# Kernel optimization log

Hardware: AMD Instinct MI355X
Metric: run time of the kernel (lower is better)

## Reference

```python
import jax, jax.numpy as jnp
import numpy as np

BINS = 256
EPS = 1e-8


def _norm255(x):
    # (x - min) / (max - min) * 255, truncated to int (torch .int())
    mx = jnp.max(x, axis=(2, 3), keepdims=True)
    mn = jnp.min(x, axis=(2, 3), keepdims=True)
    return ((x - mn) / (mx - mn) * 255.0).astype(jnp.int32)


def _hist256(x):
    # x int32 [B,C,H,W] -> per-(b,c) 256-bin histogram [B,C,256] float32
    B, C = x.shape[0], x.shape[1]
    flat = x.reshape(B * C, -1)
    rows = jnp.arange(B * C)[:, None]
    h = jnp.zeros((B * C, BINS), jnp.float32).at[rows, flat].add(1.0)
    return h.reshape(B, C, BINS)


def _entropy(x):
    # faithful to Entropy(): p = hist / (H*W); h = -sum p*log(p+1e-8)
    B, C, H, W = x.shape
    p = _hist256(x) / (H * W)
    h = -jnp.sum(p * jnp.log(p + EPS), axis=2)
    return h[:, :, None, None]  # [B,C,1,1]


def _joint_entropy(x_p, x_ms):
    # Faithful to Joint_entropy's quirky count: for each (i,j) it counts pixels
    # where (x_ms==i AND x_p==j) OR (x_ms!=i AND x_p!=j).
    # count[i,j] = 2*J[i,j] + npix - hist_ms[i] - hist_p[j], J = joint histogram.
    B, C, H, W = x_ms.shape
    npix = H * W
    bins = jnp.arange(BINS)
    M = (x_ms.reshape(B, C, npix)[..., None] == bins).astype(jnp.float32)  # [B,C,P,256]
    P = (x_p.reshape(B, npix)[..., None] == bins).astype(jnp.float32)      # [B,P,256]
    J = jnp.einsum('bcpi,bpj->bcij', M, P)                                  # [B,C,256,256]
    hist_ms = jnp.sum(M, axis=2)  # [B,C,256]
    hist_p = jnp.sum(P, axis=1)   # [B,256]
    count = 2.0 * J + npix - hist_ms[:, :, :, None] - hist_p[:, None, None, :]
    p = count / float(BINS * BINS)  # original divides by 256*256, not npix
    h = -jnp.sum(p * jnp.log(p + EPS), axis=(2, 3))
    return h[:, :, None, None]  # [B,C,1,1]


def _channel(f_p, f_ms):
    B, C, H, W = f_p.shape
    f_p_m = jnp.mean(f_p, axis=1, keepdims=True)  # [B,1,H,W]
    # AdaptiveAvgPool2d((16,16)) with H,W divisible by 16 == block mean
    pooled = f_p.reshape(B, C, 16, H // 16, 16, W // 16).mean(axis=(3, 5))
    f_p_a = jnp.mean(pooled, axis=1, keepdims=True)  # [B,1,16,16]
    f_ms_n = _norm255(f_ms)
    f_p_m_n = _norm255(f_p_m)
    f_p_a_n = _norm255(f_p_a)
    h_ms = _entropy(f_ms_n)                 # [B,C,1,1]
    h_p = _entropy(f_p_m_n)                 # [B,1,1,1]
    h_ms_p = _joint_entropy(f_p_a_n, f_ms_n)  # [B,C,1,1]
    mi = h_p + h_ms - h_ms_p
    mi = jax.nn.softmax(mi, axis=1)  # nn.Softmax() on 4D -> dim=1
    return f_ms + f_ms * mi


def _similarity(f_p, f_ms):
    B, C, H, W = f_p.shape
    f_ms_u = jax.image.resize(f_ms, (B, C, H, W), method='bilinear')
    a = f_ms_u.reshape(B, C, -1)
    b = f_p.reshape(B, C, -1)
    a = a - jnp.mean(a, axis=2, keepdims=True)
    b = b - jnp.mean(b, axis=2, keepdims=True)
    na = jnp.sqrt(jnp.sum(a * a, axis=2))  # [B,C] (ms norms)
    nb = jnp.sqrt(jnp.sum(b * b, axis=2))  # [B,C] (p norms)
    s = jnp.einsum('bcp,bdp->bcd', a, b)   # [B,C,C]
    return s / ((na * nb) / 100.0)[:, :, None]


def _spatial(f_p, f_ms):
    B, C, H, W = f_p.shape
    s_m = _similarity(f_p, f_ms)
    mx = jnp.max(s_m, axis=2)        # [B,C]
    idx = jnp.argmax(s_m, axis=2)    # [B,C] best f_p channel per ms channel
    scores = jax.nn.softmax(mx, axis=1)
    brow = jnp.arange(B)[:, None]
    # group score: sum of softmax scores of ms-channels that picked value v
    g = jnp.zeros((B, C), scores.dtype).at[brow, idx].add(scores)
    cnt = jnp.zeros((B, C), jnp.int32).at[brow, idx].add(1)
    k = jnp.min(jnp.sum(cnt > 0, axis=1))  # min #unique over batch
    min_k = (k + 1) // 2                   # ceil(min_k / 2)
    order = jnp.argsort(-g, axis=1)        # descending group score; absent groups (0) sort last
    sorted_scores = jnp.take_along_axis(g, order, axis=1)  # [B,C]
    pos_mask = jnp.arange(C) < min_k       # keep top min_k positions
    z = jnp.where(pos_mask[None, :], sorted_scores, -jnp.inf)
    w = jax.nn.softmax(z, axis=1)          # softmax over selected scores, 0 elsewhere
    gathered = jnp.take_along_axis(f_p, order[:, :, None, None], axis=1)  # [B,C,H,W]
    mask = jnp.sum(w[:, :, None, None] * jax.nn.sigmoid(gathered), axis=1, keepdims=True)
    return f_p + f_p * mask


def setup_inputs() -> dict:
    key = jax.random.key(0)
    k1, k2 = jax.random.split(key)
    f_p = jax.random.normal(k1, (8, 64, 256, 256), dtype=jnp.float32)
    f_ms = jax.random.normal(k2, (8, 64, 16, 16), dtype=jnp.float32)
    return {"f_p": f_p, "f_ms": f_ms}


def reference(f_p, f_ms):
    rel_ms = _channel(f_p, f_ms)
    rel_p = _spatial(f_p, f_ms)
    return (rel_p, rel_ms)
```

## Files before the change

### kernel.cpp

```cpp
#include <hip/hip_runtime.h>

#define BB 8
#define CC 64
#define HP 256
#define WP 256
#define PP 65536
#define QQ 256

__device__ __forceinline__ unsigned encF(float f) {
    unsigned u = __float_as_uint(f);
    return (u & 0x80000000u) ? ~u : (u | 0x80000000u);
}
__device__ __forceinline__ float decF(unsigned u) {
    unsigned b = (u & 0x80000000u) ? (u ^ 0x80000000u) : ~u;
    return __uint_as_float(b);
}

__device__ __forceinline__ double blockSumD(double v, double* red4) {
    int t = threadIdx.x;
    for (int d = 32; d; d >>= 1) v += __shfl_down(v, d, 64);
    __syncthreads();
    if ((t & 63) == 0) red4[t >> 6] = v;
    __syncthreads();
    double r = red4[0] + red4[1] + red4[2] + red4[3];
    __syncthreads();
    return r;
}

__global__ void k0_init(unsigned* minmax, int* histpm) {
    int t = threadIdx.x + blockIdx.x * blockDim.x;
    if (t < BB) { minmax[2 * t] = 0xFFFFFFFFu; minmax[2 * t + 1] = 0u; }
    if (t < BB * 256) histpm[t] = 0;
}

__global__ __launch_bounds__(256) void k1_fpm(const float* __restrict__ fp,
                                              float* __restrict__ fpm,
                                              unsigned* __restrict__ minmax) {
    int b = blockIdx.y;
    int i4 = blockIdx.x * 256 + threadIdx.x;
    const float4* src = (const float4*)(fp + (size_t)b * CC * PP);
    float sx = 0.f, sy = 0.f, sz = 0.f, sw = 0.f;
#pragma unroll 8
    for (int c = 0; c < CC; ++c) {
        float4 v = src[(size_t)c * (PP / 4) + i4];
        sx += v.x; sy += v.y; sz += v.z; sw += v.w;
    }
    const float inv = 1.0f / 64.0f;
    float4 m; m.x = sx * inv; m.y = sy * inv; m.z = sz * inv; m.w = sw * inv;
    ((float4*)(fpm + (size_t)b * PP))[i4] = m;
    float mn = fminf(fminf(m.x, m.y), fminf(m.z, m.w));
    float mx = fmaxf(fmaxf(m.x, m.y), fmaxf(m.z, m.w));
    for (int d = 32; d; d >>= 1) {
        mn = fminf(mn, __shfl_down(mn, d, 64));
        mx = fmaxf(mx, __shfl_down(mx, d, 64));
    }
    __shared__ unsigned smn, smx;
    if (threadIdx.x == 0) { smn = 0xFFFFFFFFu; smx = 0u; }
    __syncthreads();
    if ((threadIdx.x & 63) == 0) { atomicMin(&smn, encF(mn)); atomicMax(&smx, encF(mx)); }
    __syncthreads();
    if (threadIdx.x == 0) { atomicMin(&minmax[2 * b], smn); atomicMax(&minmax[2 * b + 1], smx); }
}

__global__ __launch_bounds__(256) void k2a_hist(const float* __restrict__ fpm,
                                                const unsigned* __restrict__ minmax,
                                                int* __restrict__ histpm) {
    int b = blockIdx.y;
    __shared__ int h[256];
    h[threadIdx.x] = 0;
    __syncthreads();
    float mn = decF(minmax[2 * b]);
    float mx = decF(minmax[2 * b + 1]);
    float dd = mx - mn;
    int i4 = blockIdx.x * 256 + threadIdx.x;
    float4 v = ((const float4*)(fpm + (size_t)b * PP))[i4];
    int b0 = (int)((v.x - mn) / dd * 255.0f);
    int b1 = (int)((v.y - mn) / dd * 255.0f);
    int b2 = (int)((v.z - mn) / dd * 255.0f);
    int b3 = (int)((v.w - mn) / dd * 255.0f);
    b0 = min(max(b0, 0), 255); b1 = min(max(b1, 0), 255);
    b2 = min(max(b2, 0), 255); b3 = min(max(b3, 0), 255);
    atomicAdd(&h[b0], 1); atomicAdd(&h[b1], 1);
    atomicAdd(&h[b2], 1); atomicAdd(&h[b3], 1);
    __syncthreads();
    atomicAdd(&histpm[b * 256 + threadIdx.x], h[threadIdx.x]);
}

__global__ __launch_bounds__(256) void k2b_entropy(const int* __restrict__ histpm,
                                                   float* __restrict__ hpE) {
    __shared__ double red4[4];
    int b = blockIdx.x;
    int n = histpm[b * 256 + threadIdx.x];
    float p = (float)n * (1.0f / 65536.0f);
    double term = -(double)(p * __logf(p + 1e-8f));
    double h = blockSumD(term, red4);
    if (threadIdx.x == 0) hpE[b] = (float)h;
}

__global__ __launch_bounds__(256) void k3_chan(const float* __restrict__ fp,
                                               float* __restrict__ cellsum,
                                               float* __restrict__ gtent,
                                               float* __restrict__ chsum,
                                               float* __restrict__ chsumsq) {
    int blk = blockIdx.x, b = blk >> 6, c = blk & 63;
    int x = threadIdx.x, s = x >> 4, r = x & 15;
    const float* src = fp + (size_t)(b * CC + c) * PP;
    __shared__ float tentL[256];
    __shared__ double red4[4];
    tentL[x] = 0.0f;
    __syncthreads();
    float wm, w0, wp;
    if (x <= 7)        { wm = 0.f; w0 = 1.f; wp = 0.f; }
    else if (x >= 248) { wm = 0.f; w0 = 1.f; wp = 0.f; }
    else if (r < 8)    { float fx = ((float)r + 8.5f) * 0.0625f; wm = 1.f - fx; w0 = fx;       wp = 0.f; }
    else               { float fx = ((float)r - 7.5f) * 0.0625f; wm = 0.f;      w0 = 1.f - fx; wp = fx;  }
    double sum = 0.0, ssq = 0.0;
    for (int q = 0; q < 16; ++q) {
        float am = 0.f, a0 = 0.f, ap = 0.f, cs = 0.f;
#pragma unroll
        for (int ry = 0; ry < 16; ++ry) {
            float v = src[(q * 16 + ry) * 256 + x];
            sum += (double)v;
            ssq += (double)v * (double)v;
            cs  += v;
            if ((q == 0 && ry < 8) || (q == 15 && ry >= 8)) {
                a0 += v;
            } else if (ry < 8) {
                float fy = ((float)ry + 8.5f) * 0.0625f;
                am += (1.f - fy) * v; a0 += fy * v;
            } else {
                float fy = ((float)ry - 7.5f) * 0.0625f;
                a0 += (1.f - fy) * v; ap += fy * v;
            }
        }
        float vals[10];
        vals[0] = am * wm; vals[1] = am * w0; vals[2] = am * wp;
        vals[3] = a0 * wm; vals[4] = a0 * w0; vals[5] = a0 * wp;
        vals[6] = ap * wm; vals[7] = ap * w0; vals[8] = ap * wp;
        vals[9] = cs;
#pragma unroll
        for (int d = 8; d; d >>= 1) {
#pragma unroll
            for (int k2 = 0; k2 < 10; ++k2) vals[k2] += __shfl_down(vals[k2], d, 16);
        }
        if (r == 0) {
            if (q > 0) {
                if (s > 0)  atomicAdd(&tentL[(q - 1) * 16 + (s - 1)], vals[0]);
                atomicAdd(&tentL[(q - 1) * 16 + s], vals[1]);
                if (s < 15) atomicAdd(&tentL[(q - 1) * 16 + (s + 1)], vals[2]);
            }
            if (s > 0)  atomicAdd(&tentL[q * 16 + (s - 1)], vals[3]);
            atomicAdd(&tentL[q * 16 + s], vals[4]);
            if (s < 15) atomicAdd(&tentL[q * 16 + (s + 1)], vals[5]);
            if (q < 15) {
                if (s > 0)  atomicAdd(&tentL[(q + 1) * 16 + (s - 1)], vals[6]);
                atomicAdd(&tentL[(q + 1) * 16 + s], vals[7]);
                if (s < 15) atomicAdd(&tentL[(q + 1) * 16 + (s + 1)], vals[8]);
            }
            cellsum[(size_t)(b * CC + c) * QQ + q * 16 + s] = vals[9];
        }
    }
    __syncthreads();
    gtent[(size_t)(b * CC + c) * QQ + x] = tentL[x];
    double st = blockSumD(sum, red4);
    double sq = blockSumD(ssq, red4);
    if (x == 0) { chsum[b * CC + c] = (float)st; chsumsq[b * CC + c] = (float)sq; }
}

__global__ __launch_bounds__(256) void k4_ms(const float* __restrict__ fms,
                                             int* __restrict__ msn,
                                             int* __restrict__ histms,
                                             float* __restrict__ hmsE,
                                             float* __restrict__ naArr,
                                             float* __restrict__ mssum) {
    int blk = blockIdx.x, b = blk >> 6, c = blk & 63, t = threadIdx.x;
    __shared__ float m[256];
    __shared__ int hist[256];
    __shared__ double red4[4];
    __shared__ double U[256];
    __shared__ unsigned umn, umx;
    float v = fms[(size_t)(b * CC + c) * QQ + t];
    m[t] = v;
    hist[t] = 0;
    if (t == 0) { umn = 0xFFFFFFFFu; umx = 0u; }
    float mn = v, mx = v;
    for (int d = 32; d; d >>= 1) {
        mn = fminf(mn, __shfl_down(mn, d, 64));
        mx = fmaxf(mx, __shfl_down(mx, d, 64));
    }
    __syncthreads();
    if ((t & 63) == 0) { atomicMin(&umn, encF(mn)); atomicMax(&umx, encF(mx)); }
    __syncthreads();
    mn = decF(umn); mx = decF(umx);
    int bin = (int)((v - mn) / (mx - mn) * 255.0f);
    bin = min(max(bin, 0), 255);
    msn[(size_t)(b * CC + c) * QQ + t] = bin;
    atomicAdd(&hist[bin], 1);
    __syncthreads();
    histms[(size_t)(b * CC + c) * QQ + t] = hist[t];
    float pf = (float)hist[t] * (1.0f / 256.0f);
    double term = -(double)(pf * __logf(pf + 1e-8f));
    double h = blockSumD(term, red4);
    if (t == 0) hmsE[b * CC + c] = (float)h;
    int i = t >> 4, j = t & 15;
    double kdj = (j == 0 || j == 15) ? 13.328125 : 10.65625;
    double mv = (double)m[t];
    double uu = kdj * mv + 2.671875 * ((j > 0 ? (double)m[t - 1] : 0.0) +
                                       (j < 15 ? (double)m[t + 1] : 0.0));
    U[t] = uu;
    __syncthreads();
    double kdi = (i == 0 || i == 15) ? 13.328125 : 10.65625;
    double vv = kdi * U[t] + 2.671875 * ((i > 0 ? U[t - 16] : 0.0) +
                                         (i < 15 ? U[t + 16] : 0.0));
    double sq = blockSumD(mv * vv, red4);
    double msm = blockSumD(mv, red4);
    if (t == 0) {
        mssum[b * CC + c] = (float)msm;
        double meanu = msm * (1.0 / 256.0);
        double na2 = sq - 65536.0 * meanu * meanu;
        naArr[b * CC + c] = (float)sqrt(na2 > 0.0 ? na2 : 0.0);
    }
}

__global__ __launch_bounds__(256) void k5_pa(const float* __restrict__ cellsum,
                                             int* __restrict__ pan,
                                             int* __restrict__ histp) {
    int b = blockIdx.x, t = threadIdx.x;
    __shared__ int hist[256];
    __shared__ unsigned umn, umx;
    hist[t] = 0;
    if (t == 0) { umn = 0xFFFFFFFFu; umx = 0u; }
    double acc = 0.0;
    for (int c = 0; c < CC; ++c) acc += (double)cellsum[(size_t)(b * CC + c) * QQ + t];
    float pa = (float)(acc * (1.0 / 256.0) * (1.0 / 64.0));
    float mn = pa, mx = pa;
    for (int d = 32; d; d >>= 1) {
        mn = fminf(mn, __shfl_down(mn, d, 64));
        mx = fmaxf(mx, __shfl_down(mx, d, 64));
    }
    __syncthreads();
    if ((t & 63) == 0) { atomicMin(&umn, encF(mn)); atomicMax(&umx, encF(mx)); }
    __syncthreads();
    mn = decF(umn); mx = decF(umx);
    int bin = (int)((pa - mn) / (mx - mn) * 255.0f);
    bin = min(max(bin, 0), 255);
    pan[b * QQ + t] = bin;
    atomicAdd(&hist[bin], 1);
    __syncthreads();
    histp[b * 256 + t] = hist[t];
}

__global__ __launch_bounds__(256) void k6_joint(const int* __restrict__ msn,
                                                const int* __restrict__ pan,
                                                const int* __restrict__ histms,
                                                const int* __restrict__ histp,
                                                float* __restrict__ hjoint) {
    int blk = blockIdx.x, b = blk >> 6, c = blk & 63, t = threadIdx.x;
    __shared__ int key[256], hms[256], hp[256];
    __shared__ double red4[4];
    int iv = msn[(size_t)(b * CC + c) * QQ + t];
    int jv = pan[b * QQ + t];
    key[t] = (iv << 8) | jv;
    hms[t] = histms[(size_t)(b * CC + c) * QQ + t];
    hp[t] = histp[b * 256 + t];
    __syncthreads();
    unsigned long long w0_ = 0, w1_ = 0, w2_ = 0, w3_ = 0;
    for (int p = 0; p < 256; ++p) {
        int k2 = key[p];
        if ((k2 >> 8) == t) {
            int j = k2 & 255;
            unsigned long long bit = 1ull << (j & 63);
            int w = j >> 6;
            if (w == 0) w0_ |= bit; else if (w == 1) w1_ |= bit;
            else if (w == 2) w2_ |= bit; else w3_ |= bit;
        }
    }
    double acc = 0.0;
    int basei = 256 - hms[t];
    unsigned long long words[4] = { w0_, w1_, w2_, w3_ };
#pragma unroll
    for (int w = 0; w < 4; ++w) {
        unsigned long long word = words[w];
        for (int jj = 0; jj < 64; ++jj) {
            if (!((word >> jj) & 1ull)) {
                int cnt = basei - hp[w * 64 + jj];
                float pf = (float)cnt * (1.0f / 65536.0f);
                acc -= (double)(pf * __logf(pf + 1e-8f));
            }
        }
    }
    int myk = key[t], n = 0; bool first = true;
    for (int p = 0; p < 256; ++p) {
        int k2 = key[p];
        if (k2 == myk) { n++; if (p < t) first = false; }
    }
    if (first) {
        int cnt = 2 * n + 256 - hms[myk >> 8] - hp[myk & 255];
        float pf = (float)cnt * (1.0f / 65536.0f);
        acc -= (double)(pf * __logf(pf + 1e-8f));
    }
    double h = blockSumD(acc, red4);
    if (t == 0) hjoint[b * CC + c] = (float)h;
}

__global__ __launch_bounds__(256) void k7_relms(const float* __restrict__ fms,
                                                const float* __restrict__ hmsE,
                                                const float* __restrict__ hpE,
                                                const float* __restrict__ hjoint,
                                                float* __restrict__ out2) {
    int b = blockIdx.x, t = threadIdx.x;
    __shared__ double mi[64];
    if (t < 64) mi[t] = (double)hpE[b] + (double)hmsE[b * CC + t] - (double)hjoint[b * CC + t];
    __syncthreads();
    if (t == 0) {
        double mxv = mi[0];
        for (int c2 = 1; c2 < 64; ++c2) if (mi[c2] > mxv) mxv = mi[c2];
        double s = 0.0;
        for (int c2 = 0; c2 < 64; ++c2) { mi[c2] = exp(mi[c2] - mxv); s += mi[c2]; }
        for (int c2 = 0; c2 < 64; ++c2) mi[c2] /= s;
    }
    __syncthreads();
    const float* src = fms + (size_t)b * CC * QQ;
    float* dst = out2 + (size_t)b * CC * QQ;
    for (int e = t; e < CC * QQ; e += 256) {
        float v = src[e];
        float miv = (float)mi[e >> 8];
        dst[e] = v + v * miv;
    }
}

__global__ __launch_bounds__(256) void k8_smax(const float* __restrict__ fms,
                                               const float* __restrict__ gtent,
                                               const float* __restrict__ mssum,
                                               const float* __restrict__ chsum,
                                               const float* __restrict__ chsumsq,
                                               const float* __restrict__ naArr,
                                               float* __restrict__ mxArr,
                                               int* __restrict__ idxArr) {
    int blk = blockIdx.x, b = blk >> 6, c = blk & 63, t = threadIdx.x;
    __shared__ float msrow[256];
    __shared__ double part[256];
    __shared__ double sval[64];
    msrow[t] = fms[(size_t)(b * CC + c) * QQ + t];
    __syncthreads();
    int d = t >> 2, pr = t & 3;
    const float* g = gtent + (size_t)(b * CC + d) * QQ + pr * 64;
    const float* mr = msrow + pr * 64;
    double acc = 0.0;
    for (int q2 = 0; q2 < 64; ++q2) acc += (double)mr[q2] * (double)g[q2];
    part[t] = acc;
    __syncthreads();
    if (t < 64) {
        double meanu = (double)mssum[b * CC + c] * (1.0 / 256.0);
        double meanp = (double)chsum[b * CC + t] * (1.0 / 65536.0);
        sval[t] = part[t * 4] + part[t * 4 + 1] + part[t * 4 + 2] + part[t * 4 + 3]
                  - 65536.0 * meanu * meanp;
    }
    __syncthreads();
    if (t == 0) {
        double best = sval[0]; int bi2 = 0;
        for (int dd = 1; dd < 64; ++dd) { if (sval[dd] > best) { best = sval[dd]; bi2 = dd; } }
        double nac = (double)naArr[b * CC + c];
        double sc_ = (double)chsum[b * CC + c];
        double sq_ = (double)chsumsq[b * CC + c];
        double nb2 = sq_ - sc_ * sc_ * (1.0 / 65536.0);
        double nbc = sqrt(nb2 > 0.0 ? nb2 : 0.0);
        mxArr[b * CC + c] = (float)(best * 100.0 / (nac * nbc));
        idxArr[b * CC + c] = bi2;
    }
}

__global__ __launch_bounds__(512) void k9_small(const float* __restrict__ mxArr,
                                                const int* __restrict__ idxArr,
                                                float* __restrict__ wsel,
                                                int* __restrict__ chanA,
                                                int* __restrict__ minkA) {
    __shared__ double sc[8][64];
    __shared__ double gs[8][64];
    __shared__ int idxS[8][64];
    __shared__ int ordv[8][64];
    __shared__ int uarr[8];
    __shared__ int mkS;
    int t = threadIdx.x;
    int b = t >> 6, c = t & 63;
    double v = (double)mxArr[b * 64 + c];
    double mx = v;
    for (int d = 32; d; d >>= 1) mx = fmax(mx, __shfl_down(mx, d, 64));
    mx = __shfl(mx, 0, 64);
    double e = exp(v - mx);
    double s = e;
    for (int d = 32; d; d >>= 1) s += __shfl_down(s, d, 64);
    s = __shfl(s, 0, 64);
    sc[b][c] = e / s;
    idxS[b][c] = idxArr[b * 64 + c];
    __syncthreads();
    double g = 0.0; int cnt = 0;
    for (int c2 = 0; c2 < 64; ++c2) {
        if (idxS[b][c2] == c) { g += sc[b][c2]; cnt++; }
    }
    gs[b][c] = g;
    unsigned long long ball = __ballot(cnt > 0);
    if (c == 0) uarr[b] = __popcll(ball);
    __syncthreads();
    if (t == 0) {
        int k = uarr[0];
        for (int b2 = 1; b2 < 8; ++b2) k = min(k, uarr[b2]);
        mkS = (k + 1) >> 1;
        minkA[0] = mkS;
    }
    __syncthreads();
    int rk = 0;
    double myg = gs[b][c];
    for (int c3 = 0; c3 < 64; ++c3) {
        double a = gs[b][c3];
        if (a > myg || (a == myg && c3 < c)) rk++;
    }
    ordv[b][rk] = c;
    __syncthreads();
    int mk = mkS;
    double z0 = gs[b][ordv[b][0]];
    double ee = (c < mk) ? exp(gs[b][ordv[b][c]] - z0) : 0.0;
    double se = ee;
    for (int d = 32; d; d >>= 1) se += __shfl_down(se, d, 64);
    se = __shfl(se, 0, 64);
    if (c < mk) {
        wsel[b * 64 + c] = (float)(ee / se);
        chanA[b * 64 + c] = ordv[b][c];
    }
}

__global__ __launch_bounds__(256) void k10_relp(const float* __restrict__ fp,
                                                const float* __restrict__ wsel,
                                                const int* __restrict__ chanA,
                                                const int* __restrict__ minkA,
                                                float* __restrict__ outp) {
    int b = blockIdx.y;
    int i4 = blockIdx.x * 256 + threadIdx.x;
    int mk = minkA[0];
    const float4* src = (const float4*)(fp + (size_t)b * CC * PP);
    float mx0 = 0.f, mx1 = 0.f, mx2 = 0.f, mx3 = 0.f;
    for (int i = 0; i < mk; ++i) {
        int ch = chanA[b * 64 + i];
        float wv = wsel[b * 64 + i];
        float4 v = src[(size_t)ch * (PP / 4) + i4];
        mx0 += wv * (1.0f / (1.0f + __expf(-v.x)));
        mx1 += wv * (1.0f / (1.0f + __expf(-v.y)));
        mx2 += wv * (1.0f / (1.0f + __expf(-v.z)));
        mx3 += wv * (1.0f / (1.0f + __expf(-v.w)));
    }
    float4* dst = (float4*)(outp + (size_t)b * CC * PP);
    for (int c2 = 0; c2 < CC; ++c2) {
        float4 v = src[(size_t)c2 * (PP / 4) + i4];
        float4 o;
        o.x = v.x + v.x * mx0;
        o.y = v.y + v.y * mx1;
        o.z = v.z + v.z * mx2;
        o.w = v.w + v.w * mx3;
        dst[(size_t)c2 * (PP / 4) + i4] = o;
    }
}

extern "C" void kernel_launch(void* const* d_in, const int* in_sizes, int n_in,
                              void* d_out, int out_size, void* d_ws, size_t ws_size,
                              hipStream_t stream) {
    const float* fp = (const float*)d_in[0];
    const float* fms = (const float*)d_in[1];
    float* out = (float*)d_out;

    char* p = (char*)d_ws;
    auto alloc = [&](size_t bytes) { void* r = (void*)p; p += (bytes + 255) & ~(size_t)255; return r; };

    float* fpm      = (float*)alloc((size_t)BB * PP * 4);
    float* cellsum  = (float*)alloc((size_t)BB * CC * QQ * 4);
    float* gtent    = (float*)alloc((size_t)BB * CC * QQ * 4);
    float* chsum    = (float*)alloc((size_t)BB * CC * 4);
    float* chsumsq  = (float*)alloc((size_t)BB * CC * 4);
    unsigned* minmax= (unsigned*)alloc((size_t)BB * 2 * 4);
    int* histpm     = (int*)alloc((size_t)BB * 256 * 4);
    int* msn        = (int*)alloc((size_t)BB * CC * QQ * 4);
    int* histms     = (int*)alloc((size_t)BB * CC * 256 * 4);
    int* histp      = (int*)alloc((size_t)BB * 256 * 4);
    int* pan        = (int*)alloc((size_t)BB * QQ * 4);
    float* hmsE     = (float*)alloc((size_t)BB * CC * 4);
    float* hpE      = (float*)alloc((size_t)BB * 4);
    float* hjoint   = (float*)alloc((size_t)BB * CC * 4);
    float* naArr    = (float*)alloc((size_t)BB * CC * 4);
    float* mssum    = (float*)alloc((size_t)BB * CC * 4);
    float* mxArr    = (float*)alloc((size_t)BB * CC * 4);
    int* idxArr     = (int*)alloc((size_t)BB * CC * 4);
    float* wsel     = (float*)alloc((size_t)BB * CC * 4);
    int* chanA      = (int*)alloc((size_t)BB * CC * 4);
    int* minkA      = (int*)alloc(256);

    float* out_relp  = out;
    float* out_relms = out + (size_t)BB * CC * PP;

    k0_init<<<8, 256, 0, stream>>>(minmax, histpm);
    k1_fpm<<<dim3(64, 8), 256, 0, stream>>>(fp, fpm, minmax);
    k2a_hist<<<dim3(64, 8), 256, 0, stream>>>(fpm, minmax, histpm);
    k2b_entropy<<<8, 256, 0, stream>>>(histpm, hpE);
    k3_chan<<<512, 256, 0, stream>>>(fp, cellsum, gtent, chsum, chsumsq);
    k4_ms<<<512, 256, 0, stream>>>(fms, msn, histms, hmsE, naArr, mssum);
    k5_pa<<<8, 256, 0, stream>>>(cellsum, pan, histp);
    k6_joint<<<512, 256, 0, stream>>>(msn, pan, histms, histp, hjoint);
    k7_relms<<<8, 256, 0, stream>>>(fms, hmsE, hpE, hjoint, out_relms);
    k8_smax<<<512, 256, 0, stream>>>(fms, gtent, mssum, chsum, chsumsq, naArr, mxArr, idxArr);
    k9_small<<<1, 512, 0, stream>>>(mxArr, idxArr, wsel, chanA, minkA);
    k10_relp<<<dim3(64, 8), 256, 0, stream>>>(fp, wsel, chanA, minkA, out_relp);
}
```

Measured before the change: 416.7 us.

## Fuse channel-mean and per-channel statistics into a single pass over f_p

The previous code read f_p twice before the final output pass: once for the channel mean and once for per-channel tent sums, cell sums and moments. This change merges both into one kernel that tiles over (batch, row-band, channel-group) and builds the mean with global float atomics, with channel sums accumulated as double atomics. Several small kernels (f_ms stats, histogram/entropy, softmax vs. smax) are also merged to cut launch count. The cost is many global atomics, which make the float sums order-nondeterministic, plus an extra zeroing pass over the fpm and gtent buffers.

Result: slower. 447.3 us (+7.3%).

```diff
diff --git a/kernel.cpp b/kernel.cpp
--- a/kernel.cpp
+++ b/kernel.cpp
@@ -27,27 +27,206 @@
     return r;
 }
 
-__global__ void k0_init(unsigned* minmax, int* histpm) {
-    int t = threadIdx.x + blockIdx.x * blockDim.x;
+__global__ __launch_bounds__(256) void k0_zero(float* __restrict__ fpm,
+                                               float* __restrict__ gtent,
+                                               double* __restrict__ chsumD,
+                                               double* __restrict__ chsumsqD,
+                                               unsigned* __restrict__ minmax) {
+    int t = blockIdx.x * 256 + threadIdx.x;
+    ((float2*)fpm)[t] = make_float2(0.f, 0.f);
+    if (t < BB * CC * QQ) gtent[t] = 0.f;
+    if (t < BB * CC) { chsumD[t] = 0.0; chsumsqD[t] = 0.0; }
     if (t < BB) { minmax[2 * t] = 0xFFFFFFFFu; minmax[2 * t + 1] = 0u; }
-    if (t < BB * 256) histpm[t] = 0;
-}
-
-__global__ __launch_bounds__(256) void k1_fpm(const float* __restrict__ fp,
-                                              float* __restrict__ fpm,
-                                              unsigned* __restrict__ minmax) {
+}
+
+__global__ __launch_bounds__(256) void kA_fused(const float* __restrict__ fp,
+                                                const float* __restrict__ fms,
+                                                float* __restrict__ fpm,
+                                                float* __restrict__ cellsum,
+                                                float* __restrict__ gtent,
+                                                double* __restrict__ chsumD,
+                                                double* __restrict__ chsumsqD,
+                                                int* __restrict__ msn,
+                                                int* __restrict__ histms,
+                                                float* __restrict__ hmsE,
+                                                float* __restrict__ naArr,
+                                                float* __restrict__ mssum) {
+    int blk = blockIdx.x;
+    if (blk < 512) {
+        int b = blk >> 6, q = (blk >> 2) & 15, g = blk & 3;
+        int x = threadIdx.x;
+        int cg = x >> 2, rg = x & 3;
+        int col0 = cg * 4;
+        int s = x >> 4, r = x & 15;
+        float wxm[4], wx0[4], wxp[4];
+#pragma unroll
+        for (int cc = 0; cc < 4; ++cc) {
+            int col = col0 + cc; int rr = col & 15;
+            if (col <= 7 || col >= 248)      { wxm[cc] = 0.f; wx0[cc] = 1.f; wxp[cc] = 0.f; }
+            else if (rr < 8) { float fx = ((float)rr + 8.5f) * 0.0625f; wxm[cc] = 1.f - fx; wx0[cc] = fx;       wxp[cc] = 0.f; }
+            else             { float fx = ((float)rr - 7.5f) * 0.0625f; wxm[cc] = 0.f;      wx0[cc] = 1.f - fx; wxp[cc] = fx; }
+        }
+        float wym[4], wy0[4], wyp[4];
+#pragma unroll
+        for (int rr = 0; rr < 4; ++rr) {
+            int ry = rg * 4 + rr;
+            if ((q == 0 && ry < 8) || (q == 15 && ry >= 8)) { wym[rr] = 0.f; wy0[rr] = 1.f; wyp[rr] = 0.f; }
+            else if (ry < 8) { float fy = ((float)ry + 8.5f) * 0.0625f; wym[rr] = 1.f - fy; wy0[rr] = fy;       wyp[rr] = 0.f; }
+            else             { float fy = ((float)ry - 7.5f) * 0.0625f; wym[rr] = 0.f;      wy0[rr] = 1.f - fy; wyp[rr] = fy; }
+        }
+        float4 acc0 = make_float4(0.f, 0.f, 0.f, 0.f);
+        float4 acc1 = acc0, acc2 = acc0, acc3 = acc0;
+        const float* base = fp + (size_t)(b * CC + g * 16) * PP
+                               + (size_t)(q * 16 + rg * 4) * WP + col0;
+#pragma unroll 4
+        for (int c = 0; c < 16; ++c) {
+            const float* srcp = base + (size_t)c * PP;
+            float4 v0 = *(const float4*)(srcp);
+            float4 v1 = *(const float4*)(srcp + WP);
+            float4 v2 = *(const float4*)(srcp + 2 * WP);
+            float4 v3 = *(const float4*)(srcp + 3 * WP);
+
+            acc0.x += v0.x; acc0.y += v0.y; acc0.z += v0.z; acc0.w += v0.w;
+            acc1.x += v1.x; acc1.y += v1.y; acc1.z += v1.z; acc1.w += v1.w;
+            acc2.x += v2.x; acc2.y += v2.y; acc2.z += v2.z; acc2.w += v2.w;
+            acc3.x += v3.x; acc3.y += v3.y; acc3.z += v3.z; acc3.w += v3.w;
+
+            float amx = wym[0]*v0.x + wym[1]*v1.x + wym[2]*v2.x + wym[3]*v3.x;
+            float amy = wym[0]*v0.y + wym[1]*v1.y + wym[2]*v2.y + wym[3]*v3.y;
+            float amz = wym[0]*v0.z + wym[1]*v1.z + wym[2]*v2.z + wym[3]*v3.z;
+            float amw = wym[0]*v0.w + wym[1]*v1.w + wym[2]*v2.w + wym[3]*v3.w;
+            float a0x = wy0[0]*v0.x + wy0[1]*v1.x + wy0[2]*v2.x + wy0[3]*v3.x;
+            float a0y = wy0[0]*v0.y + wy0[1]*v1.y + wy0[2]*v2.y + wy0[3]*v3.y;
+            float a0z = wy0[0]*v0.z + wy0[1]*v1.z + wy0[2]*v2.z + wy0[3]*v3.z;
+            float a0w = wy0[0]*v0.w + wy0[1]*v1.w + wy0[2]*v2.w + wy0[3]*v3.w;
+            float apx = wyp[0]*v0.x + wyp[1]*v1.x + wyp[2]*v2.x + wyp[3]*v3.x;
+            float apy = wyp[0]*v0.y + wyp[1]*v1.y + wyp[2]*v2.y + wyp[3]*v3.y;
+            float apz = wyp[0]*v0.z + wyp[1]*v1.z + wyp[2]*v2.z + wyp[3]*v3.z;
+            float apw = wyp[0]*v0.w + wyp[1]*v1.w + wyp[2]*v2.w + wyp[3]*v3.w;
+
+            float csx = v0.x + v1.x + v2.x + v3.x;
+            float csy = v0.y + v1.y + v2.y + v3.y;
+            float csz = v0.z + v1.z + v2.z + v3.z;
+            float csw = v0.w + v1.w + v2.w + v3.w;
+            float cs = csx + csy + csz + csw;
+            float sq = v0.x*v0.x + v0.y*v0.y + v0.z*v0.z + v0.w*v0.w
+                     + v1.x*v1.x + v1.y*v1.y + v1.z*v1.z + v1.w*v1.w
+                     + v2.x*v2.x + v2.y*v2.y + v2.z*v2.z + v2.w*v2.w
+                     + v3.x*v3.x + v3.y*v3.y + v3.z*v3.z + v3.w*v3.w;
+
+            float vals[10];
+            vals[0] = amx*wxm[0] + amy*wxm[1] + amz*wxm[2] + amw*wxm[3];
+            vals[1] = amx*wx0[0] + amy*wx0[1] + amz*wx0[2] + amw*wx0[3];
+            vals[2] = amx*wxp[0] + amy*wxp[1] + amz*wxp[2] + amw*wxp[3];
+            vals[3] = a0x*wxm[0] + a0y*wxm[1] + a0z*wxm[2] + a0w*wxm[3];
+            vals[4] = a0x*wx0[0] + a0y*wx0[1] + a0z*wx0[2] + a0w*wx0[3];
+            vals[5] = a0x*wxp[0] + a0y*wxp[1] + a0z*wxp[2] + a0w*wxp[3];
+            vals[6] = apx*wxm[0] + apy*wxm[1] + apz*wxm[2] + apw*wxm[3];
+            vals[7] = apx*wx0[0] + apy*wx0[1] + apz*wx0[2] + apw*wx0[3];
+            vals[8] = apx*wxp[0] + apy*wxp[1] + apz*wxp[2] + apw*wxp[3];
+            vals[9] = cs;
+#pragma unroll
+            for (int d = 8; d; d >>= 1) {
+#pragma unroll
+                for (int k2 = 0; k2 < 10; ++k2) vals[k2] += __shfl_down(vals[k2], d, 16);
+            }
+            int ch = g * 16 + c;
+            if (r == 0) {
+                float* gt = gtent + (size_t)(b * CC + ch) * QQ;
+                if (q > 0) {
+                    if (s > 0)  atomicAdd(&gt[(q - 1) * 16 + (s - 1)], vals[0]);
+                    atomicAdd(&gt[(q - 1) * 16 + s], vals[1]);
+                    if (s < 15) atomicAdd(&gt[(q - 1) * 16 + (s + 1)], vals[2]);
+                }
+                if (s > 0)  atomicAdd(&gt[q * 16 + (s - 1)], vals[3]);
+                atomicAdd(&gt[q * 16 + s], vals[4]);
+                if (s < 15) atomicAdd(&gt[q * 16 + (s + 1)], vals[5]);
+                if (q < 15) {
+                    if (s > 0)  atomicAdd(&gt[(q + 1) * 16 + (s - 1)], vals[6]);
+                    atomicAdd(&gt[(q + 1) * 16 + s], vals[7]);
+                    if (s < 15) atomicAdd(&gt[(q + 1) * 16 + (s + 1)], vals[8]);
+                }
+                cellsum[(size_t)(b * CC + ch) * QQ + q * 16 + s] = vals[9];
+            }
+            double csD = (double)cs, sqD = (double)sq;
+            for (int d = 32; d; d >>= 1) {
+                csD += __shfl_down(csD, d, 64);
+                sqD += __shfl_down(sqD, d, 64);
+            }
+            if ((x & 63) == 0) {
+                atomicAdd(&chsumD[b * CC + ch], csD);
+                atomicAdd(&chsumsqD[b * CC + ch], sqD);
+            }
+        }
+        float* fb = fpm + (size_t)b * PP + (size_t)(q * 16 + rg * 4) * WP + col0;
+        atomicAdd(&fb[0], acc0.x); atomicAdd(&fb[1], acc0.y);
+        atomicAdd(&fb[2], acc0.z); atomicAdd(&fb[3], acc0.w);
+        atomicAdd(&fb[WP + 0], acc1.x); atomicAdd(&fb[WP + 1], acc1.y);
+        atomicAdd(&fb[WP + 2], acc1.z); atomicAdd(&fb[WP + 3], acc1.w);
+        atomicAdd(&fb[2 * WP + 0], acc2.x); atomicAdd(&fb[2 * WP + 1], acc2.y);
+        atomicAdd(&fb[2 * WP + 2], acc2.z); atomicAdd(&fb[2 * WP + 3], acc2.w);
+        atomicAdd(&fb[3 * WP + 0], acc3.x); atomicAdd(&fb[3 * WP + 1], acc3.y);
+        atomicAdd(&fb[3 * WP + 2], acc3.z); atomicAdd(&fb[3 * WP + 3], acc3.w);
+    } else {
+        int blk2 = blk - 512, b = blk2 >> 6, c = blk2 & 63, t = threadIdx.x;
+        __shared__ float m[256];
+        __shared__ int hist[256];
+        __shared__ double red4[4];
+        __shared__ double U[256];
+        __shared__ unsigned umn, umx;
+        float v = fms[(size_t)(b * CC + c) * QQ + t];
+        m[t] = v;
+        hist[t] = 0;
+        if (t == 0) { umn = 0xFFFFFFFFu; umx = 0u; }
+        float mn = v, mx = v;
+        for (int d = 32; d; d >>= 1) {
+            mn = fminf(mn, __shfl_down(mn, d, 64));
+            mx = fmaxf(mx, __shfl_down(mx, d, 64));
+        }
+        __syncthreads();
+        if ((t & 63) == 0) { atomicMin(&umn, encF(mn)); atomicMax(&umx, encF(mx)); }
+        __syncthreads();
+        mn = decF(umn); mx = decF(umx);
+        int bin = (int)((v - mn) / (mx - mn) * 255.0f);
+        bin = min(max(bin, 0), 255);
+        msn[(size_t)(b * CC + c) * QQ + t] = bin;
+        atomicAdd(&hist[bin], 1);
+        __syncthreads();
+        histms[(size_t)(b * CC + c) * QQ + t] = hist[t];
+        float pf = (float)hist[t] * (1.0f / 256.0f);
+        double term = -(double)(pf * __logf(pf + 1e-8f));
+        double h = blockSumD(term, red4);
+        if (t == 0) hmsE[b * CC + c] = (float)h;
+        int i = t >> 4, j = t & 15;
+        double kdj = (j == 0 || j == 15) ? 13.328125 : 10.65625;
+        double mv = (double)m[t];
+        double uu = kdj * mv + 2.671875 * ((j > 0 ? (double)m[t - 1] : 0.0) +
+                                           (j < 15 ? (double)m[t + 1] : 0.0));
+        U[t] = uu;
+        __syncthreads();
+        double kdi = (i == 0 || i == 15) ? 13.328125 : 10.65625;
+        double vv = kdi * U[t] + 2.671875 * ((i > 0 ? U[t - 16] : 0.0) +
+                                             (i < 15 ? U[t + 16] : 0.0));
+        double sqv = blockSumD(mv * vv, red4);
+        double msm = blockSumD(mv, red4);
+        if (t == 0) {
+            mssum[b * CC + c] = (float)msm;
+            double meanu = msm * (1.0 / 256.0);
+            double na2 = sqv - 65536.0 * meanu * meanu;
+            naArr[b * CC + c] = (float)sqrt(na2 > 0.0 ? na2 : 0.0);
+        }
+    }
+}
+
+__global__ __launch_bounds__(256) void kB_finish(float* __restrict__ fpm,
+                                                 unsigned* __restrict__ minmax) {
     int b = blockIdx.y;
     int i4 = blockIdx.x * 256 + threadIdx.x;
-    const float4* src = (const float4*)(fp + (size_t)b * CC * PP);
-    float sx = 0.f, sy = 0.f, sz = 0.f, sw = 0.f;
-#pragma unroll 8
-    for (int c = 0; c < CC; ++c) {
-        float4 v = src[(size_t)c * (PP / 4) + i4];
-        sx += v.x; sy += v.y; sz += v.z; sw += v.w;
-    }
+    float4* p4 = (float4*)(fpm + (size_t)b * PP);
+    float4 m = p4[i4];
     const float inv = 1.0f / 64.0f;
-    float4 m; m.x = sx * inv; m.y = sy * inv; m.z = sz * inv; m.w = sw * inv;
-    ((float4*)(fpm + (size_t)b * PP))[i4] = m;
+    m.x *= inv; m.y *= inv; m.z *= inv; m.w *= inv;
+    p4[i4] = m;
     float mn = fminf(fminf(m.x, m.y), fminf(m.z, m.w));
     float mx = fmaxf(fmaxf(m.x, m.y), fmaxf(m.z, m.w));
     for (int d = 32; d; d >>= 1) {
@@ -62,187 +241,56 @@
     if (threadIdx.x == 0) { atomicMin(&minmax[2 * b], smn); atomicMax(&minmax[2 * b + 1], smx); }
 }
 
-__global__ __launch_bounds__(256) void k2a_hist(const float* __restrict__ fpm,
+__global__ __launch_bounds__(256) void kC_small(const float* __restrict__ fpm,
                                                 const unsigned* __restrict__ minmax,
-                                                int* __restrict__ histpm) {
-    int b = blockIdx.y;
-    __shared__ int h[256];
-    h[threadIdx.x] = 0;
+                                                const float* __restrict__ cellsum,
+                                                float* __restrict__ hpE,
+                                                int* __restrict__ pan,
+                                                int* __restrict__ histp) {
+    int b = blockIdx.x, t = threadIdx.x;
+    __shared__ int hist[256];
+    __shared__ double red4[4];
+    __shared__ unsigned umn, umx;
+    hist[t] = 0;
+    if (t == 0) { umn = 0xFFFFFFFFu; umx = 0u; }
     __syncthreads();
     float mn = decF(minmax[2 * b]);
     float mx = decF(minmax[2 * b + 1]);
     float dd = mx - mn;
-    int i4 = blockIdx.x * 256 + threadIdx.x;
-    float4 v = ((const float4*)(fpm + (size_t)b * PP))[i4];
-    int b0 = (int)((v.x - mn) / dd * 255.0f);
-    int b1 = (int)((v.y - mn) / dd * 255.0f);
-    int b2 = (int)((v.z - mn) / dd * 255.0f);
-    int b3 = (int)((v.w - mn) / dd * 255.0f);
-    b0 = min(max(b0, 0), 255); b1 = min(max(b1, 0), 255);
-    b2 = min(max(b2, 0), 255); b3 = min(max(b3, 0), 255);
-    atomicAdd(&h[b0], 1); atomicAdd(&h[b1], 1);
-    atomicAdd(&h[b2], 1); atomicAdd(&h[b3], 1);
-    __syncthreads();
-    atomicAdd(&histpm[b * 256 + threadIdx.x], h[threadIdx.x]);
-}
-
-__global__ __launch_bounds__(256) void k2b_entropy(const int* __restrict__ histpm,
-                                                   float* __restrict__ hpE) {
-    __shared__ double red4[4];
-    int b = blockIdx.x;
-    int n = histpm[b * 256 + threadIdx.x];
+    const float4* src = (const float4*)(fpm + (size_t)b * PP);
+    for (int i4 = t; i4 < PP / 4; i4 += 256) {
+        float4 v = src[i4];
+        int b0 = (int)((v.x - mn) / dd * 255.0f);
+        int b1 = (int)((v.y - mn) / dd * 255.0f);
+        int b2 = (int)((v.z - mn) / dd * 255.0f);
+        int b3 = (int)((v.w - mn) / dd * 255.0f);
+        b0 = min(max(b0, 0), 255); b1 = min(max(b1, 0), 255);
+        b2 = min(max(b2, 0), 255); b3 = min(max(b3, 0), 255);
+        atomicAdd(&hist[b0], 1); atomicAdd(&hist[b1], 1);
+        atomicAdd(&hist[b2], 1); atomicAdd(&hist[b3], 1);
+    }
+    __syncthreads();
+    int n = hist[t];
     float p = (float)n * (1.0f / 65536.0f);
     double term = -(double)(p * __logf(p + 1e-8f));
     double h = blockSumD(term, red4);
-    if (threadIdx.x == 0) hpE[b] = (float)h;
-}
-
-__global__ __launch_bounds__(256) void k3_chan(const float* __restrict__ fp,
-                                               float* __restrict__ cellsum,
-                                               float* __restrict__ gtent,
-                                               float* __restrict__ chsum,
-                                               float* __restrict__ chsumsq) {
-    int blk = blockIdx.x, b = blk >> 6, c = blk & 63;
-    int x = threadIdx.x, s = x >> 4, r = x & 15;
-    const float* src = fp + (size_t)(b * CC + c) * PP;
-    __shared__ float tentL[256];
-    __shared__ double red4[4];
-    tentL[x] = 0.0f;
-    __syncthreads();
-    float wm, w0, wp;
-    if (x <= 7)        { wm = 0.f; w0 = 1.f; wp = 0.f; }
-    else if (x >= 248) { wm = 0.f; w0 = 1.f; wp = 0.f; }
-    else if (r < 8)    { float fx = ((float)r + 8.5f) * 0.0625f; wm = 1.f - fx; w0 = fx;       wp = 0.f; }
-    else               { float fx = ((float)r - 7.5f) * 0.0625f; wm = 0.f;      w0 = 1.f - fx; wp = fx;  }
-    double sum = 0.0, ssq = 0.0;
-    for (int q = 0; q < 16; ++q) {
-        float am = 0.f, a0 = 0.f, ap = 0.f, cs = 0.f;
-#pragma unroll
-        for (int ry = 0; ry < 16; ++ry) {
-            float v = src[(q * 16 + ry) * 256 + x];
-            sum += (double)v;
-            ssq += (double)v * (double)v;
-            cs  += v;
-            if ((q == 0 && ry < 8) || (q == 15 && ry >= 8)) {
-                a0 += v;
-            } else if (ry < 8) {
-                float fy = ((float)ry + 8.5f) * 0.0625f;
-                am += (1.f - fy) * v; a0 += fy * v;
-            } else {
-                float fy = ((float)ry - 7.5f) * 0.0625f;
-                a0 += (1.f - fy) * v; ap += fy * v;
-            }
-        }
-        float vals[10];
-        vals[0] = am * wm; vals[1] = am * w0; vals[2] = am * wp;
-        vals[3] = a0 * wm; vals[4] = a0 * w0; vals[5] = a0 * wp;
-        vals[6] = ap * wm; vals[7] = ap * w0; vals[8] = ap * wp;
-        vals[9] = cs;
-#pragma unroll
-        for (int d = 8; d; d >>= 1) {
-#pragma unroll
-            for (int k2 = 0; k2 < 10; ++k2) vals[k2] += __shfl_down(vals[k2], d, 16);
-        }
-        if (r == 0) {
-            if (q > 0) {
-                if (s > 0)  atomicAdd(&tentL[(q - 1) * 16 + (s - 1)], vals[0]);
-                atomicAdd(&tentL[(q - 1) * 16 + s], vals[1]);
-                if (s < 15) atomicAdd(&tentL[(q - 1) * 16 + (s + 1)], vals[2]);
-            }
-            if (s > 0)  atomicAdd(&tentL[q * 16 + (s - 1)], vals[3]);
-            atomicAdd(&tentL[q * 16 + s], vals[4]);
-            if (s < 15) atomicAdd(&tentL[q * 16 + (s + 1)], vals[5]);
-            if (q < 15) {
-                if (s > 0)  atomicAdd(&tentL[(q + 1) * 16 + (s - 1)], vals[6]);
-                atomicAdd(&tentL[(q + 1) * 16 + s], vals[7]);
-                if (s < 15) atomicAdd(&tentL[(q + 1) * 16 + (s + 1)], vals[8]);
-            }
-            cellsum[(size_t)(b * CC + c) * QQ + q * 16 + s] = vals[9];
-        }
-    }
-    __syncthreads();
-    gtent[(size_t)(b * CC + c) * QQ + x] = tentL[x];
-    double st = blockSumD(sum, red4);
-    double sq = blockSumD(ssq, red4);
-    if (x == 0) { chsum[b * CC + c] = (float)st; chsumsq[b * CC + c] = (float)sq; }
-}
-
-__global__ __launch_bounds__(256) void k4_ms(const float* __restrict__ fms,
-                                             int* __restrict__ msn,
-                                             int* __restrict__ histms,
-                                             float* __restrict__ hmsE,
-                                             float* __restrict__ naArr,
-                                             float* __restrict__ mssum) {
-    int blk = blockIdx.x, b = blk >> 6, c = blk & 63, t = threadIdx.x;
-    __shared__ float m[256];
-    __shared__ int hist[256];
-    __shared__ double red4[4];
-    __shared__ double U[256];
-    __shared__ unsigned umn, umx;
-    float v = fms[(size_t)(b * CC + c) * QQ + t];
-    m[t] = v;
+    if (t == 0) hpE[b] = (float)h;
+    __syncthreads();
     hist[t] = 0;
-    if (t == 0) { umn = 0xFFFFFFFFu; umx = 0u; }
-    float mn = v, mx = v;
-    for (int d = 32; d; d >>= 1) {
-        mn = fminf(mn, __shfl_down(mn, d, 64));
-        mx = fmaxf(mx, __shfl_down(mx, d, 64));
-    }
-    __syncthreads();
-    if ((t & 63) == 0) { atomicMin(&umn, encF(mn)); atomicMax(&umx, encF(mx)); }
-    __syncthreads();
-    mn = decF(umn); mx = decF(umx);
-    int bin = (int)((v - mn) / (mx - mn) * 255.0f);
-    bin = min(max(bin, 0), 255);
-    msn[(size_t)(b * CC + c) * QQ + t] = bin;
-    atomicAdd(&hist[bin], 1);
-    __syncthreads();
-    histms[(size_t)(b * CC + c) * QQ + t] = hist[t];
-    float pf = (float)hist[t] * (1.0f / 256.0f);
-    double term = -(double)(pf * __logf(pf + 1e-8f));
-    double h = blockSumD(term, red4);
-    if (t == 0) hmsE[b * CC + c] = (float)h;
-    int i = t >> 4, j = t & 15;
-    double kdj = (j == 0 || j == 15) ? 13.328125 : 10.65625;
-    double mv = (double)m[t];
-    double uu = kdj * mv + 2.671875 * ((j > 0 ? (double)m[t - 1] : 0.0) +
-                                       (j < 15 ? (double)m[t + 1] : 0.0));
-    U[t] = uu;
-    __syncthreads();
-    double kdi = (i == 0 || i == 15) ? 13.328125 : 10.65625;
-    double vv = kdi * U[t] + 2.671875 * ((i > 0 ? U[t - 16] : 0.0) +
-                                         (i < 15 ? U[t + 16] : 0.0));
-    double sq = blockSumD(mv * vv, red4);
-    double msm = blockSumD(mv, red4);
-    if (t == 0) {
-        mssum[b * CC + c] = (float)msm;
-        double meanu = msm * (1.0 / 256.0);
-        double na2 = sq - 65536.0 * meanu * meanu;
-        naArr[b * CC + c] = (float)sqrt(na2 > 0.0 ? na2 : 0.0);
-    }
-}
-
-__global__ __launch_bounds__(256) void k5_pa(const float* __restrict__ cellsum,
-                                             int* __restrict__ pan,
-                                             int* __restrict__ histp) {
-    int b = blockIdx.x, t = threadIdx.x;
-    __shared__ int hist[256];
-    __shared__ unsigned umn, umx;
-    hist[t] = 0;
-    if (t == 0) { umn = 0xFFFFFFFFu; umx = 0u; }
+    __syncthreads();
     double acc = 0.0;
     for (int c = 0; c < CC; ++c) acc += (double)cellsum[(size_t)(b * CC + c) * QQ + t];
     float pa = (float)(acc * (1.0 / 256.0) * (1.0 / 64.0));
-    float mn = pa, mx = pa;
+    float mn2 = pa, mx2 = pa;
     for (int d = 32; d; d >>= 1) {
-        mn = fminf(mn, __shfl_down(mn, d, 64));
-        mx = fmaxf(mx, __shfl_down(mx, d, 64));
-    }
-    __syncthreads();
-    if ((t & 63) == 0) { atomicMin(&umn, encF(mn)); atomicMax(&umx, encF(mx)); }
-    __syncthreads();
-    mn = decF(umn); mx = decF(umx);
-    int bin = (int)((pa - mn) / (mx - mn) * 255.0f);
+        mn2 = fminf(mn2, __shfl_down(mn2, d, 64));
+        mx2 = fmaxf(mx2, __shfl_down(mx2, d, 64));
+    }
+    __syncthreads();
+    if ((t & 63) == 0) { atomicMin(&umn, encF(mn2)); atomicMax(&umx, encF(mx2)); }
+    __syncthreads();
+    mn2 = decF(umn); mx2 = decF(umx);
+    int bin = (int)((pa - mn2) / (mx2 - mn2) * 255.0f);
     bin = min(max(bin, 0), 255);
     pan[b * QQ + t] = bin;
     atomicAdd(&hist[bin], 1);
@@ -303,70 +351,71 @@
     if (t == 0) hjoint[b * CC + c] = (float)h;
 }
 
-__global__ __launch_bounds__(256) void k7_relms(const float* __restrict__ fms,
+__global__ __launch_bounds__(256) void kE_fused(const float* __restrict__ fms,
+                                                const float* __restrict__ gtent,
+                                                const float* __restrict__ mssum,
+                                                const double* __restrict__ chsumD,
+                                                const double* __restrict__ chsumsqD,
+                                                const float* __restrict__ naArr,
                                                 const float* __restrict__ hmsE,
                                                 const float* __restrict__ hpE,
                                                 const float* __restrict__ hjoint,
+                                                float* __restrict__ mxArr,
+                                                int* __restrict__ idxArr,
                                                 float* __restrict__ out2) {
-    int b = blockIdx.x, t = threadIdx.x;
-    __shared__ double mi[64];
-    if (t < 64) mi[t] = (double)hpE[b] + (double)hmsE[b * CC + t] - (double)hjoint[b * CC + t];
-    __syncthreads();
-    if (t == 0) {
-        double mxv = mi[0];
-        for (int c2 = 1; c2 < 64; ++c2) if (mi[c2] > mxv) mxv = mi[c2];
-        double s = 0.0;
-        for (int c2 = 0; c2 < 64; ++c2) { mi[c2] = exp(mi[c2] - mxv); s += mi[c2]; }
-        for (int c2 = 0; c2 < 64; ++c2) mi[c2] /= s;
-    }
-    __syncthreads();
-    const float* src = fms + (size_t)b * CC * QQ;
-    float* dst = out2 + (size_t)b * CC * QQ;
-    for (int e = t; e < CC * QQ; e += 256) {
-        float v = src[e];
-        float miv = (float)mi[e >> 8];
-        dst[e] = v + v * miv;
-    }
-}
-
-__global__ __launch_bounds__(256) void k8_smax(const float* __restrict__ fms,
-                                               const float* __restrict__ gtent,
-                                               const float* __restrict__ mssum,
-                                               const float* __restrict__ chsum,
-                                               const float* __restrict__ chsumsq,
-                                               const float* __restrict__ naArr,
-                                               float* __restrict__ mxArr,
-                                               int* __restrict__ idxArr) {
-    int blk = blockIdx.x, b = blk >> 6, c = blk & 63, t = threadIdx.x;
-    __shared__ float msrow[256];
-    __shared__ double part[256];
-    __shared__ double sval[64];
-    msrow[t] = fms[(size_t)(b * CC + c) * QQ + t];
-    __syncthreads();
-    int d = t >> 2, pr = t & 3;
-    const float* g = gtent + (size_t)(b * CC + d) * QQ + pr * 64;
-    const float* mr = msrow + pr * 64;
-    double acc = 0.0;
-    for (int q2 = 0; q2 < 64; ++q2) acc += (double)mr[q2] * (double)g[q2];
-    part[t] = acc;
-    __syncthreads();
-    if (t < 64) {
-        double meanu = (double)mssum[b * CC + c] * (1.0 / 256.0);
-        double meanp = (double)chsum[b * CC + t] * (1.0 / 65536.0);
-        sval[t] = part[t * 4] + part[t * 4 + 1] + part[t * 4 + 2] + part[t * 4 + 3]
-                  - 65536.0 * meanu * meanp;
-    }
-    __syncthreads();
-    if (t == 0) {
-        double best = sval[0]; int bi2 = 0;
-        for (int dd = 1; dd < 64; ++dd) { if (sval[dd] > best) { best = sval[dd]; bi2 = dd; } }
-        double nac = (double)naArr[b * CC + c];
-        double sc_ = (double)chsum[b * CC + c];
-        double sq_ = (double)chsumsq[b * CC + c];
-        double nb2 = sq_ - sc_ * sc_ * (1.0 / 65536.0);
-        double nbc = sqrt(nb2 > 0.0 ? nb2 : 0.0);
-        mxArr[b * CC + c] = (float)(best * 100.0 / (nac * nbc));
-        idxArr[b * CC + c] = bi2;
+    int blk = blockIdx.x;
+    if (blk < 512) {
+        int b = blk >> 6, c = blk & 63, t = threadIdx.x;
+        __shared__ float msrow[256];
+        __shared__ double part[256];
+        __shared__ double sval[64];
+        msrow[t] = fms[(size_t)(b * CC + c) * QQ + t];
+        __syncthreads();
+        int d = t >> 2, pr = t & 3;
+        const float* g = gtent + (size_t)(b * CC + d) * QQ + pr * 64;
+        const float* mr = msrow + pr * 64;
+        double acc = 0.0;
+        for (int q2 = 0; q2 < 64; ++q2) acc += (double)mr[q2] * (double)g[q2];
+        part[t] = acc;
+        __syncthreads();
+        if (t < 64) {
+            double meanu = (double)mssum[b * CC + c] * (1.0 / 256.0);
+            double meanp = chsumD[b * CC + t] * (1.0 / 65536.0);
+            sval[t] = part[t * 4] + part[t * 4 + 1] + part[t * 4 + 2] + part[t * 4 + 3]
+                      - 65536.0 * meanu * meanp;
+        }
+        __syncthreads();
+        if (t == 0) {
+            double best = sval[0]; int bi2 = 0;
+            for (int dd = 1; dd < 64; ++dd) { if (sval[dd] > best) { best = sval[dd]; bi2 = dd; } }
+            double nac = (double)naArr[b * CC + c];
+            double sc_ = chsumD[b * CC + c];
+            double sq_ = chsumsqD[b * CC + c];
+            double nb2 = sq_ - sc_ * sc_ * (1.0 / 65536.0);
+            double nbc = sqrt(nb2 > 0.0 ? nb2 : 0.0);
+            mxArr[b * CC + c] = (float)(best * 100.0 / (nac * nbc));
+            idxArr[b * CC + c] = bi2;
+        }
+    } else {
+        int b = blk - 512, t = threadIdx.x;
+        __shared__ double mi[64];
+        if (t < 64) mi[t] = (double)hpE[b] + (double)hmsE[b * CC + t] - (double)hjoint[b * CC + t];
+        __syncthreads();
+        if (t == 0) {
+            double mxv = mi[0];
+            for (int c2 = 1; c2 < 64; ++c2) if (mi[c2] > mxv) mxv = mi[c2];
+            double sum = 0.0;
+            for (int c2 = 0; c2 < 64; ++c2) { mi[c2] = exp(mi[c2] - mxv); sum += mi[c2]; }
+            for (int c2 = 0; c2 < 64; ++c2) mi[c2] /= sum;
+        }
+        __syncthreads();
+        const float* src = fms + (size_t)b * CC * QQ;
+        float* dst = out2 + (size_t)b * CC * QQ;
+        for (int e = t; e < CC * QQ; e += 256) {
+            float v = src[e];
+            float miv = (float)mi[e >> 8];
+            dst[e] = v + v * miv;
+        }
     }
 }
 
@@ -473,10 +522,9 @@
     float* fpm      = (float*)alloc((size_t)BB * PP * 4);
     float* cellsum  = (float*)alloc((size_t)BB * CC * QQ * 4);
     float* gtent    = (float*)alloc((size_t)BB * CC * QQ * 4);
-    float* chsum    = (float*)alloc((size_t)BB * CC * 4);
-    float* chsumsq  = (float*)alloc((size_t)BB * CC * 4);
+    double* chsumD  = (double*)alloc((size_t)BB * CC * 8);
+    double* chsumsqD= (double*)alloc((size_t)BB * CC * 8);
     unsigned* minmax= (unsigned*)alloc((size_t)BB * 2 * 4);
-    int* histpm     = (int*)alloc((size_t)BB * 256 * 4);
     int* msn        = (int*)alloc((size_t)BB * CC * QQ * 4);
     int* histms     = (int*)alloc((size_t)BB * CC * 256 * 4);
     int* histp      = (int*)alloc((size_t)BB * 256 * 4);
@@ -495,16 +543,14 @@
     float* out_relp  = out;
     float* out_relms = out + (size_t)BB * CC * PP;
 
-    k0_init<<<8, 256, 0, stream>>>(minmax, histpm);
-    k1_fpm<<<dim3(64, 8), 256, 0, stream>>>(fp, fpm, minmax);
-    k2a_hist<<<dim3(64, 8), 256, 0, stream>>>(fpm, minmax, histpm);
-    k2b_entropy<<<8, 256, 0, stream>>>(histpm, hpE);
-    k3_chan<<<512, 256, 0, stream>>>(fp, cellsum, gtent, chsum, chsumsq);
-    k4_ms<<<512, 256, 0, stream>>>(fms, msn, histms, hmsE, naArr, mssum);
-    k5_pa<<<8, 256, 0, stream>>>(cellsum, pan, histp);
+    k0_zero<<<1024, 256, 0, stream>>>(fpm, gtent, chsumD, chsumsqD, minmax);
+    kA_fused<<<1024, 256, 0, stream>>>(fp, fms, fpm, cellsum, gtent, chsumD, chsumsqD,
+                                       msn, histms, hmsE, naArr, mssum);
+    kB_finish<<<dim3(64, 8), 256, 0, stream>>>(fpm, minmax);
+    kC_small<<<8, 256, 0, stream>>>(fpm, minmax, cellsum, hpE, pan, histp);
     k6_joint<<<512, 256, 0, stream>>>(msn, pan, histms, histp, hjoint);
-    k7_relms<<<8, 256, 0, stream>>>(fms, hmsE, hpE, hjoint, out_relms);
-    k8_smax<<<512, 256, 0, stream>>>(fms, gtent, mssum, chsum, chsumsq, naArr, mxArr, idxArr);
+    kE_fused<<<520, 256, 0, stream>>>(fms, gtent, mssum, chsumD, chsumsqD, naArr,
+                                      hmsE, hpE, hjoint, mxArr, idxArr, out_relms);
     k9_small<<<1, 512, 0, stream>>>(mxArr, idxArr, wsel, chanA, minkA);
     k10_relp<<<dim3(64, 8), 256, 0, stream>>>(fp, wsel, chanA, minkA, out_relp);
 }
```
